# Kernel tuning notes

Hardware: AMD Instinct MI355X
Metric: run time of the kernel (lower is better)

Reference implementation:

```python
import jax, jax.numpy as jnp
import numpy as np

# ---- constants from the module ----
E_L, E_e, E_i = -65.0, 0.0, -80.0
V_th, V_reset, V_floor = -50.0, -65.0, -200.0
dt = 0.25
T_STEPS = 4000
DECAY_AMPA = float(np.exp(-dt / 2.0))   # tau_ampa = 2.0
DECAY_GABA = float(np.exp(-dt / 9.0))   # tau_gaba = 9.0
C_M_E, G_L_E = 1.0, 1.0 / 20.0          # tau_m_E = 20
C_M_I, G_L_I = 0.5, 0.5 / 5.0           # tau_m_I = 5
REF_E = 12                               # round(3.0/0.25)
REF_I = 6                                # round(1.5/0.25)
CM_BACK = 80.0
SLOPE = 1.0                              # biophysical surrogate slope

@jax.custom_vjp
def spike(u):
    # Heaviside forward, fast-sigmoid surrogate backward (SurrogateSpike)
    return (u >= 0).astype(u.dtype)

def _spike_fwd(u):
    return (u >= 0).astype(u.dtype), u

def _spike_bwd(u, g):
    return (g * SLOPE / (1.0 + SLOPE * jnp.abs(u)) ** 2,)

spike.defvjp(_spike_fwd, _spike_bwd)

def _scale_grad(x, scale):
    # forward identity, gradient scaled by `scale`
    return x * scale + jax.lax.stop_gradient(x) * (1.0 - scale)

def lif_step(v, I_total, ref, C_m, g_L, ref_steps):
    dv = (dt / C_m) * (-g_L * (v - E_L) + I_total)
    dv = _scale_grad(dv, 1.0 / CM_BACK)
    v = jnp.maximum(v + dv, V_floor)
    ref = jnp.maximum(ref - 1, 0)
    can_spike = ref == 0
    s = spike(v - V_th) * can_spike.astype(v.dtype)
    spiked_or_ref = (s > 0) | ~can_spike
    v = jnp.where(spiked_or_ref, V_reset, v)
    ref = jnp.where(s > 0, ref_steps, ref)
    return v, s, ref

def setup_inputs() -> dict:
    key = jax.random.key(0)
    ks = jax.random.split(key, 6)
    T, B, N_IN, N_E, N_I, N_OUT = T_STEPS, 64, 64, 256, 64, 10

    def init_w(k, shape, mean, std):
        # init_weight: N(mean,std) clamped >=0, fan-in normalized
        w = jnp.maximum(jax.random.normal(k, shape, jnp.float32) * std + mean, 0.0)
        return w / shape[0]

    return {
        "input_spikes": (jax.random.uniform(ks[0], (T, B, N_IN)) < 0.02).astype(jnp.float32),
        "W_ff0": init_w(ks[1], (N_IN, N_E), 5.1, 3.8),
        "W_ff1": init_w(ks[2], (N_E, N_OUT), 5.1, 3.8),
        "W_ee": init_w(ks[3], (N_E, N_E), 0.0, 0.0),
        "W_ei": init_w(ks[4], (N_E, N_I), 1.0, 0.5),
        "W_ie": init_w(ks[5], (N_I, N_E), 3.0, 1.5),
    }

def reference(input_spikes, W_ff0, W_ff1, W_ee, W_ei, W_ie):
    # Dale's law: feedforward weights clamped >= 0 in forward
    W0 = jnp.maximum(W_ff0, 0.0)
    W1 = jnp.maximum(W_ff1, 0.0)
    B = input_spikes.shape[1]
    N_E, N_I, N_OUT = W0.shape[1], W_ei.shape[1], W1.shape[1]
    f32 = input_spikes.dtype

    z = lambda n: jnp.zeros((B, n), f32)
    vl = lambda n: jnp.full((B, n), E_L, f32)
    zr = lambda n: jnp.zeros((B, n), jnp.int32)

    carry0 = (vl(N_E), zr(N_E), z(N_E), z(N_E), z(N_E),   # E pop: v, ref, g_ampa, g_gaba, spikes
              vl(N_I), zr(N_I), z(N_I), z(N_I),           # I pop: v, ref, g_ampa, spikes
              vl(N_OUT), zr(N_OUT), z(N_OUT),             # out pop: v, ref, g_ampa
              z(N_OUT))                                    # output spike accumulator

    def step(c, s_in):
        v_e, r_e, ge_e, gi_e, s_e, v_i, r_i, ge_i, s_i, v_o, r_o, g_o, acc = c
        # exp_synapse: spike kicks first, then decay
        ge_e = (ge_e + s_in @ W0 + s_e @ W_ee) * DECAY_AMPA
        gi_e = (gi_e + s_i @ W_ie) * DECAY_GABA
        ge_i = (ge_i + s_e @ W_ei) * DECAY_AMPA
        # E neurons: COBA with excitation + inhibition
        v_e, s_e, r_e = lif_step(v_e, ge_e * (E_e - v_e) + gi_e * (E_i - v_e), r_e, C_M_E, G_L_E, REF_E)
        # I neurons: COBA excitation only
        v_i, s_i, r_i = lif_step(v_i, ge_i * (E_e - v_i), r_i, C_M_I, G_L_I, REF_I)
        # output layer driven by fresh E spikes
        g_o = (g_o + s_e @ W1) * DECAY_AMPA
        v_o, s_o, r_o = lif_step(v_o, g_o * (E_e - v_o), r_o, C_M_E, G_L_E, REF_E)
        acc = acc + s_o
        return (v_e, r_e, ge_e, gi_e, s_e, v_i, r_i, ge_i, s_i, v_o, r_o, g_o, acc), None

    cT, _ = jax.lax.scan(step, carry0, input_spikes)
    return cT[-1]  # [B, N_OUT] output spike counts over T_steps
```

## Files before the change

### kernel.cpp

```cpp
#include <hip/hip_runtime.h>
#include <math.h>

#pragma clang fp contract(off)

#define BB 64
#define N_IN 64
#define N_E 256
#define N_I 64
#define N_OUT 10

__device__ inline unsigned long long rfl64(unsigned long long x) {
  unsigned int lo = __builtin_amdgcn_readfirstlane((unsigned int)x);
  unsigned int hi = __builtin_amdgcn_readfirstlane((unsigned int)(x >> 32));
  return (((unsigned long long)hi) << 32) | (unsigned long long)lo;
}

__global__ __launch_bounds__(256, 1) void ping_kernel(
    const float* __restrict__ g_in,
    const float* __restrict__ g_W0,
    const float* __restrict__ g_W1,
    const float* __restrict__ g_Wee,
    const float* __restrict__ g_Wei,
    const float* __restrict__ g_Wie,
    float* __restrict__ g_out,
    int T, float dA, float dG)
{
  const int tid  = threadIdx.x;
  const int lane = tid & 63;
  const int wav  = tid >> 6;
  const int b    = blockIdx.x;
  const int col  = (lane < N_OUT) ? lane : 0;

  __shared__ float sWie[N_I * N_E];
  __shared__ float sWei[N_E * N_I];
  __shared__ float sW1[N_E * N_OUT];
  __shared__ float sZeroRow[256];
  __shared__ float sP[2][4][64];
  __shared__ float sKo[2][4][16];
  __shared__ unsigned sTag[2][4];
  __shared__ unsigned long long sME[2][4];
  __shared__ int sWee;

  {
    const float4* s0 = (const float4*)g_Wie; float4* d0 = (float4*)sWie;
    for (int k = tid; k < (N_I * N_E) / 4; k += 256) d0[k] = s0[k];
    const float4* s1 = (const float4*)g_Wei; float4* d1 = (float4*)sWei;
    for (int k = tid; k < (N_E * N_I) / 4; k += 256) d1[k] = s1[k];
    for (int k = tid; k < N_E * N_OUT; k += 256) sW1[k] = fmaxf(g_W1[k], 0.f);
  }
  sZeroRow[tid] = 0.f;
  if (tid < 4) { sME[0][tid] = 0ull; sME[1][tid] = 0ull; }
  if (tid < 8) sTag[tid >> 2][tid & 3] = 0u;
  if (tid == 0) sWee = 0;
  {
    bool any = false;
    const float4* p = (const float4*)g_Wee;
    for (int k = tid; k < (N_E * N_E) / 4; k += 256) {
      float4 x = p[k];
      any |= (x.x != 0.f) | (x.y != 0.f) | (x.z != 0.f) | (x.w != 0.f);
    }
    if (__ballot(any) != 0ull && lane == 0) sWee = 1;
  }
  __syncthreads();
  const int wee = sWee;

  float vE = -65.f, ge = 0.f, gi = 0.f; int rE = 0;
  float vI = -65.f, gI = 0.f; int rI = 0;
  float vO = -65.f, gO = 0.f, accO = 0.f; int rO = 0;

  unsigned long long mE = 0ull;
  unsigned long long mI = 0ull;
  unsigned long long we0 = 0ull, we1 = 0ull, we2 = 0ull, we3 = 0ull;

  float cur = g_in[b * N_IN + lane];
  float n1  = g_in[((T > 1 ? 1 : 0) * BB + b) * N_IN + lane];

  unsigned long long mInC = __ballot(cur != 0.f);
  unsigned long long aRemC = 0ull;
  bool vaC[4] = {false, false, false, false};
  float fwC[4];
  if (mInC) {
    unsigned long long a = mInC;
    int ja[4];
#pragma unroll
    for (int k = 0; k < 4; ++k) {
      vaC[k] = (a != 0ull); ja[k] = vaC[k] ? (__ffsll(a) - 1) : 0; a &= (a - 1ull);
    }
    aRemC = a;
#pragma unroll
    for (int k = 0; k < 4; ++k) fwC[k] = g_W0[ja[k] * N_E + tid];
  }

  for (int t = 0; t < T; ++t) {
    const int slot = t & 1;
    const int tp = (t + 2 < T) ? (t + 2) : (T - 1);
    float n2 = g_in[(tp * BB + b) * N_IN + lane];

    float pEI = 0.f, kow = 0.f;
    {
      unsigned long long e = mE;
      const int base = wav * 64;
      while (e) {
        const float *qb[4], *rb[4];
#pragma unroll
        for (int k = 0; k < 4; ++k) {
          bool v = (e != 0ull); int j = v ? (__ffsll(e) - 1) : 0; e &= (e - 1ull);
          qb[k] = v ? &sWei[(base + j) * N_I] : sZeroRow;
          rb[k] = v ? &sW1[(base + j) * N_OUT] : sZeroRow;
        }
        float fq[4], fr[4];
#pragma unroll
        for (int k = 0; k < 4; ++k) { fq[k] = qb[k][lane]; fr[k] = rb[k][col]; }
#pragma unroll
        for (int k = 0; k < 4; ++k) pEI += fq[k];
#pragma unroll
        for (int k = 0; k < 4; ++k) kow += fr[k];
      }
    }

    sP[slot][wav][lane] = pEI;
    if (lane < 16) sKo[slot][wav][lane] = kow;
    asm volatile("s_waitcnt lgkmcnt(0)" ::: "memory");
    if (lane == 0) *((volatile unsigned*)&sTag[slot][wav]) = (unsigned)(t + 1);

    float kie = 0.f;
    {
      unsigned long long c = mI;
      while (c) {
        const float* pb[8];
#pragma unroll
        for (int k = 0; k < 8; ++k) {
          bool v = (c != 0ull); int j = v ? (__ffsll(c) - 1) : 0; c &= (c - 1ull);
          pb[k] = v ? &sWie[j * N_E] : sZeroRow;
        }
        float fI[8];
#pragma unroll
        for (int k = 0; k < 8; ++k) fI[k] = pb[k][tid];
#pragma unroll
        for (int k = 0; k < 8; ++k) kie += fI[k];
      }
    }

    float kin = 0.f;
    if (mInC) {
#pragma unroll
      for (int k = 0; k < 4; ++k) kin += vaC[k] ? fmaxf(fwC[k], 0.f) : 0.f;
      while (aRemC) {
        int j = __ffsll(aRemC) - 1; aRemC &= (aRemC - 1ull);
        kin += fmaxf(g_W0[j * N_E + tid], 0.f);
      }
    }

    float kee = 0.f;
    if (wee) {
      unsigned long long m0 = we0, m1 = we1, m2 = we2, m3 = we3;
      while (m0 | m1 | m2 | m3) {
        bool h0 = (m0 != 0ull), h1 = (m1 != 0ull), h2 = (m2 != 0ull), h3 = (m3 != 0ull);
        int idx = 0;
        if (h0)      { idx = __ffsll(m0) - 1;       m0 &= (m0 - 1ull); }
        else if (h1) { idx = 64 + __ffsll(m1) - 1;  m1 &= (m1 - 1ull); }
        else if (h2) { idx = 128 + __ffsll(m2) - 1; m2 &= (m2 - 1ull); }
        else if (h3) { idx = 192 + __ffsll(m3) - 1; m3 &= (m3 - 1ull); }
        kee += g_Wee[idx * N_E + tid];
      }
    }

    ge = ((ge + kin) + kee) * dA;
    gi = (gi + kie) * dG;
    {
      float t2 = ge * (0.f - vE);
      float t3 = gi * (-80.f - vE);
      float Itot = t2 + t3;
      float dv = 0.25f * ((-0.05f) * (vE - (-65.f)) + Itot);
      dv = dv * 0.0125f + dv * 0.9875f;
      vE = fmaxf(vE + dv, -200.f);
      rE = rE - 1; if (rE < 0) rE = 0;
      bool can = (rE == 0);
      bool sE = ((vE - (-50.f)) >= 0.f) && can;
      vE = (sE || !can) ? -65.f : vE;
      rE = sE ? 12 : rE;
      unsigned long long fresh = __ballot(sE);
      if (wee && lane == 0) sME[slot][wav] = fresh;
      mE = fresh;
    }

    {
      const unsigned want = (unsigned)(t + 1);
      volatile unsigned* vt = &sTag[slot][0];
      while (true) {
        unsigned a0 = vt[0], a1 = vt[1], a2 = vt[2], a3 = vt[3];
        if ((((a0 ^ want) | (a1 ^ want)) | ((a2 ^ want) | (a3 ^ want))) == 0u) break;
      }
      asm volatile("" ::: "memory");
    }

    float p0 = sP[slot][0][lane], p1 = sP[slot][1][lane];
    float p2 = sP[slot][2][lane], p3 = sP[slot][3][lane];
    float k0 = sKo[slot][0][col], k1 = sKo[slot][1][col];
    float k2 = sKo[slot][2][col], k3 = sKo[slot][3][col];

    {
      float p = ((p0 + p1) + p2) + p3;
      gI = (gI + p) * dA;
      float Ii = gI * (0.f - vI);
      float dvi = 0.5f * ((-0.1f) * (vI - (-65.f)) + Ii);
      dvi = dvi * 0.0125f + dvi * 0.9875f;
      vI = fmaxf(vI + dvi, -200.f);
      rI = rI - 1; if (rI < 0) rI = 0;
      bool canI = (rI == 0);
      bool sI = ((vI - (-50.f)) >= 0.f) && canI;
      vI = (sI || !canI) ? -65.f : vI;
      rI = sI ? 6 : rI;
      mI = __ballot(sI);
    }

    {
      float ko = ((k0 + k1) + k2) + k3;
      gO = (gO + ko) * dA;
      float Io = gO * (0.f - vO);
      float dvo = 0.25f * ((-0.05f) * (vO - (-65.f)) + Io);
      dvo = dvo * 0.0125f + dvo * 0.9875f;
      vO = fmaxf(vO + dvo, -200.f);
      rO = rO - 1; if (rO < 0) rO = 0;
      bool canO = (rO == 0);
      bool sO = ((vO - (-50.f)) >= 0.f) && canO;
      vO = (sO || !canO) ? -65.f : vO;
      rO = sO ? 12 : rO;
      accO += sO ? 1.f : 0.f;
    }

    if (wee) {
      __syncthreads();
      we0 = rfl64(sME[slot][0]); we1 = rfl64(sME[slot][1]);
      we2 = rfl64(sME[slot][2]); we3 = rfl64(sME[slot][3]);
    }

    mInC = __ballot(n1 != 0.f);
    aRemC = 0ull;
    vaC[0] = vaC[1] = vaC[2] = vaC[3] = false;
    if (mInC) {
      unsigned long long a = mInC;
      int ja[4];
#pragma unroll
      for (int k = 0; k < 4; ++k) {
        vaC[k] = (a != 0ull); ja[k] = vaC[k] ? (__ffsll(a) - 1) : 0; a &= (a - 1ull);
      }
      aRemC = a;
#pragma unroll
      for (int k = 0; k < 4; ++k) fwC[k] = g_W0[ja[k] * N_E + tid];
    }

    cur = n1; n1 = n2;
  }

  {
    float kd = 0.f;
    unsigned long long e = mE;
    const int base = wav * 64;
    while (e) {
      const float* rb[4];
#pragma unroll
      for (int k = 0; k < 4; ++k) {
        bool v = (e != 0ull); int j = v ? (__ffsll(e) - 1) : 0; e &= (e - 1ull);
        rb[k] = v ? &sW1[(base + j) * N_OUT] : sZeroRow;
      }
      float fr[4];
#pragma unroll
      for (int k = 0; k < 4; ++k) fr[k] = rb[k][col];
#pragma unroll
      for (int k = 0; k < 4; ++k) kd += fr[k];
    }
    __syncthreads();
    sP[0][wav][lane] = kd;
    __syncthreads();
    float ko = ((sP[0][0][col] + sP[0][1][col]) + sP[0][2][col]) + sP[0][3][col];
    gO = (gO + ko) * dA;
    float Io = gO * (0.f - vO);
    float dvo = 0.25f * ((-0.05f) * (vO - (-65.f)) + Io);
    dvo = dvo * 0.0125f + dvo * 0.9875f;
    vO = fmaxf(vO + dvo, -200.f);
    rO = rO - 1; if (rO < 0) rO = 0;
    bool canO = (rO == 0);
    bool sO = ((vO - (-50.f)) >= 0.f) && canO;
    accO += sO ? 1.f : 0.f;
  }

  if (wav == 0 && lane < N_OUT) g_out[b * N_OUT + lane] = accO;
}

extern "C" void kernel_launch(void* const* d_in, const int* in_sizes, int n_in,
                              void* d_out, int out_size, void* d_ws, size_t ws_size,
                              hipStream_t stream) {
  const float* g_in  = (const float*)d_in[0];
  const float* g_W0  = (const float*)d_in[1];
  const float* g_W1  = (const float*)d_in[2];
  const float* g_Wee = (const float*)d_in[3];
  const float* g_Wei = (const float*)d_in[4];
  const float* g_Wie = (const float*)d_in[5];
  float* out = (float*)d_out;
  int T = in_sizes[0] / (BB * N_IN);
  float dA = (float)exp(-0.25 / 2.0);
  float dG = (float)exp(-0.25 / 9.0);
  ping_kernel<<<dim3(BB), dim3(256), 0, stream>>>(g_in, g_W0, g_W1, g_Wee, g_Wei, g_Wie, out, T, dA, dG);
}
```

Before: 5.295 ms.

## Software-pipeline E-spike and I-spike LDS gathers into the previous iteration

Moves the gathers of Wei/W1 rows for fresh E spikes and of Wie rows for fresh I spikes so they are issued right after the spike ballots, overlapping the LDS latency with the inter-wave spin wait and the remaining neuron updates. The partial sums are carried across iterations (pEI_nx, kow_nx, kieF) and published at the start of the next step. The input-spike W0 prefetch is also moved earlier. This raises register pressure and changes the order of the float additions for pEI, which could shift results in rare cases.

```diff
diff --git a/kernel.cpp b/kernel.cpp
--- a/kernel.cpp
+++ b/kernel.cpp
@@ -72,6 +72,10 @@
   unsigned long long mI = 0ull;
   unsigned long long we0 = 0ull, we1 = 0ull, we2 = 0ull, we3 = 0ull;
 
+  float pEI_nx = 0.f, kow_nx = 0.f;
+  float kieF[8] = {0,0,0,0,0,0,0,0};
+  unsigned long long kieRem = 0ull;
+
   float cur = g_in[b * N_IN + lane];
   float n1  = g_in[((T > 1 ? 1 : 0) * BB + b) * N_IN + lane];
 
@@ -96,49 +100,26 @@
     const int tp = (t + 2 < T) ? (t + 2) : (T - 1);
     float n2 = g_in[(tp * BB + b) * N_IN + lane];
 
-    float pEI = 0.f, kow = 0.f;
-    {
-      unsigned long long e = mE;
-      const int base = wav * 64;
-      while (e) {
-        const float *qb[4], *rb[4];
-#pragma unroll
-        for (int k = 0; k < 4; ++k) {
-          bool v = (e != 0ull); int j = v ? (__ffsll(e) - 1) : 0; e &= (e - 1ull);
-          qb[k] = v ? &sWei[(base + j) * N_I] : sZeroRow;
-          rb[k] = v ? &sW1[(base + j) * N_OUT] : sZeroRow;
-        }
-        float fq[4], fr[4];
-#pragma unroll
-        for (int k = 0; k < 4; ++k) { fq[k] = qb[k][lane]; fr[k] = rb[k][col]; }
-#pragma unroll
-        for (int k = 0; k < 4; ++k) pEI += fq[k];
-#pragma unroll
-        for (int k = 0; k < 4; ++k) kow += fr[k];
-      }
-    }
-
-    sP[slot][wav][lane] = pEI;
-    if (lane < 16) sKo[slot][wav][lane] = kow;
+    sP[slot][wav][lane] = pEI_nx;
+    if (lane < 16) sKo[slot][wav][lane] = kow_nx;
     asm volatile("s_waitcnt lgkmcnt(0)" ::: "memory");
     if (lane == 0) *((volatile unsigned*)&sTag[slot][wav]) = (unsigned)(t + 1);
 
     float kie = 0.f;
-    {
-      unsigned long long c = mI;
-      while (c) {
-        const float* pb[8];
-#pragma unroll
-        for (int k = 0; k < 8; ++k) {
-          bool v = (c != 0ull); int j = v ? (__ffsll(c) - 1) : 0; c &= (c - 1ull);
-          pb[k] = v ? &sWie[j * N_E] : sZeroRow;
-        }
-        float fI[8];
-#pragma unroll
-        for (int k = 0; k < 8; ++k) fI[k] = pb[k][tid];
-#pragma unroll
-        for (int k = 0; k < 8; ++k) kie += fI[k];
-      }
+#pragma unroll
+    for (int k = 0; k < 8; ++k) kie += kieF[k];
+    while (kieRem) {
+      const float* pb[4];
+#pragma unroll
+      for (int k = 0; k < 4; ++k) {
+        bool v = (kieRem != 0ull); int j = v ? (__ffsll(kieRem) - 1) : 0; kieRem &= (kieRem - 1ull);
+        pb[k] = v ? &sWie[j * N_E] : sZeroRow;
+      }
+      float fI[4];
+#pragma unroll
+      for (int k = 0; k < 4; ++k) fI[k] = pb[k][tid];
+#pragma unroll
+      for (int k = 0; k < 4; ++k) kie += fI[k];
     }
 
     float kin = 0.f;
@@ -184,6 +165,38 @@
       mE = fresh;
     }
 
+    float fqN[6], frN[6];
+    unsigned long long eRem;
+    {
+      unsigned long long e = mE;
+      const int base = wav * 64;
+      const float *qb[6], *rb[6];
+#pragma unroll
+      for (int k = 0; k < 6; ++k) {
+        bool v = (e != 0ull); int j = v ? (__ffsll(e) - 1) : 0; e &= (e - 1ull);
+        qb[k] = v ? &sWei[(base + j) * N_I] : sZeroRow;
+        rb[k] = v ? &sW1[(base + j) * N_OUT] : sZeroRow;
+      }
+      eRem = e;
+#pragma unroll
+      for (int k = 0; k < 6; ++k) { fqN[k] = qb[k][lane]; frN[k] = rb[k][col]; }
+    }
+
+    mInC = __ballot(n1 != 0.f);
+    aRemC = 0ull;
+    vaC[0] = vaC[1] = vaC[2] = vaC[3] = false;
+    if (mInC) {
+      unsigned long long a = mInC;
+      int ja[4];
+#pragma unroll
+      for (int k = 0; k < 4; ++k) {
+        vaC[k] = (a != 0ull); ja[k] = vaC[k] ? (__ffsll(a) - 1) : 0; a &= (a - 1ull);
+      }
+      aRemC = a;
+#pragma unroll
+      for (int k = 0; k < 4; ++k) fwC[k] = g_W0[ja[k] * N_E + tid];
+    }
+
     {
       const unsigned want = (unsigned)(t + 1);
       volatile unsigned* vt = &sTag[slot][0];
@@ -215,6 +228,19 @@
     }
 
     {
+      unsigned long long c = mI;
+      const float* pb[8];
+#pragma unroll
+      for (int k = 0; k < 8; ++k) {
+        bool v = (c != 0ull); int j = v ? (__ffsll(c) - 1) : 0; c &= (c - 1ull);
+        pb[k] = v ? &sWie[j * N_E] : sZeroRow;
+      }
+      kieRem = c;
+#pragma unroll
+      for (int k = 0; k < 8; ++k) kieF[k] = pb[k][tid];
+    }
+
+    {
       float ko = ((k0 + k1) + k2) + k3;
       gO = (gO + ko) * dA;
       float Io = gO * (0.f - vO);
@@ -235,19 +261,30 @@
       we2 = rfl64(sME[slot][2]); we3 = rfl64(sME[slot][3]);
     }
 
-    mInC = __ballot(n1 != 0.f);
-    aRemC = 0ull;
-    vaC[0] = vaC[1] = vaC[2] = vaC[3] = false;
-    if (mInC) {
-      unsigned long long a = mInC;
-      int ja[4];
-#pragma unroll
-      for (int k = 0; k < 4; ++k) {
-        vaC[k] = (a != 0ull); ja[k] = vaC[k] ? (__ffsll(a) - 1) : 0; a &= (a - 1ull);
-      }
-      aRemC = a;
-#pragma unroll
-      for (int k = 0; k < 4; ++k) fwC[k] = g_W0[ja[k] * N_E + tid];
+    {
+      float pe = 0.f, ko2 = 0.f;
+#pragma unroll
+      for (int k = 0; k < 6; ++k) pe += fqN[k];
+#pragma unroll
+      for (int k = 0; k < 6; ++k) ko2 += frN[k];
+      const int base = wav * 64;
+      while (eRem) {
+        const float *qb[4], *rb[4];
+#pragma unroll
+        for (int k = 0; k < 4; ++k) {
+          bool v = (eRem != 0ull); int j = v ? (__ffsll(eRem) - 1) : 0; eRem &= (eRem - 1ull);
+          qb[k] = v ? &sWei[(base + j) * N_I] : sZeroRow;
+          rb[k] = v ? &sW1[(base + j) * N_OUT] : sZeroRow;
+        }
+        float fq[4], fr[4];
+#pragma unroll
+        for (int k = 0; k < 4; ++k) { fq[k] = qb[k][lane]; fr[k] = rb[k][col]; }
+#pragma unroll
+        for (int k = 0; k < 4; ++k) pe += fq[k];
+#pragma unroll
+        for (int k = 0; k < 4; ++k) ko2 += fr[k];
+      }
+      pEI_nx = pe; kow_nx = ko2;
     }
 
     cur = n1; n1 = n2;
```

Result: slower. 5.990 ms (+13.1%).

## Interleave Wei and W1 rows in shared memory and specialize loop on Wee

Applied to the files above, without the earlier changes.

Merges the E→I and E→output weight tables into one padded 80-wide shared-memory row per excitatory neuron, so each spiking neuron's contributions come from a single computed row pointer. The time loop is split into two specialized versions depending on whether W_ee is nonzero, removing the per-step wee branches and the recurrent-E machinery in the common zero case. It also moves the next-input mask preparation ahead of the spin-wait and polls the four wave tags with two 64-bit loads instead of four 32-bit loads. Costs are duplicated code and a serial per-thread global-to-shared copy during setup instead of vectorized float4 copies.

```diff
diff --git a/kernel.cpp b/kernel.cpp
--- a/kernel.cpp
+++ b/kernel.cpp
@@ -30,23 +30,27 @@
   const int wav  = tid >> 6;
   const int b    = blockIdx.x;
   const int col  = (lane < N_OUT) ? lane : 0;
+  const int colO = 64 + col;
 
   __shared__ float sWie[N_I * N_E];
-  __shared__ float sWei[N_E * N_I];
-  __shared__ float sW1[N_E * N_OUT];
+  __shared__ float sWeiO[N_E * 80];
   __shared__ float sZeroRow[256];
   __shared__ float sP[2][4][64];
   __shared__ float sKo[2][4][16];
-  __shared__ unsigned sTag[2][4];
+  __shared__ __align__(16) unsigned sTag[2][4];
   __shared__ unsigned long long sME[2][4];
   __shared__ int sWee;
 
   {
     const float4* s0 = (const float4*)g_Wie; float4* d0 = (float4*)sWie;
     for (int k = tid; k < (N_I * N_E) / 4; k += 256) d0[k] = s0[k];
-    const float4* s1 = (const float4*)g_Wei; float4* d1 = (float4*)sWei;
-    for (int k = tid; k < (N_E * N_I) / 4; k += 256) d1[k] = s1[k];
-    for (int k = tid; k < N_E * N_OUT; k += 256) sW1[k] = fmaxf(g_W1[k], 0.f);
+    {
+      int j = tid;
+      float* row = &sWeiO[j * 80];
+      for (int c = 0; c < 64; ++c) row[c] = g_Wei[j * N_I + c];
+      for (int o = 0; o < N_OUT; ++o) row[64 + o] = fmaxf(g_W1[j * N_OUT + o], 0.f);
+      for (int c = 74; c < 80; ++c) row[c] = 0.f;
+    }
   }
   sZeroRow[tid] = 0.f;
   if (tid < 4) { sME[0][tid] = 0ull; sME[1][tid] = 0ull; }
@@ -70,7 +74,6 @@
 
   unsigned long long mE = 0ull;
   unsigned long long mI = 0ull;
-  unsigned long long we0 = 0ull, we1 = 0ull, we2 = 0ull, we3 = 0ull;
 
   float cur = g_in[b * N_IN + lane];
   float n1  = g_in[((T > 1 ? 1 : 0) * BB + b) * N_IN + lane];
@@ -91,182 +94,321 @@
     for (int k = 0; k < 4; ++k) fwC[k] = g_W0[ja[k] * N_E + tid];
   }
 
-  for (int t = 0; t < T; ++t) {
-    const int slot = t & 1;
-    const int tp = (t + 2 < T) ? (t + 2) : (T - 1);
-    float n2 = g_in[(tp * BB + b) * N_IN + lane];
-
-    float pEI = 0.f, kow = 0.f;
-    {
-      unsigned long long e = mE;
-      const int base = wav * 64;
-      while (e) {
-        const float *qb[4], *rb[4];
+  const int base64 = wav * 64;
+
+  if (!wee) {
+    for (int t = 0; t < T; ++t) {
+      const int slot = t & 1;
+      const int tp = (t + 2 < T) ? (t + 2) : (T - 1);
+      float n2 = g_in[(tp * BB + b) * N_IN + lane];
+
+      float pEI = 0.f, kow = 0.f;
+      {
+        unsigned long long e = mE;
+        while (e) {
+          const float* qb[4];
+#pragma unroll
+          for (int k = 0; k < 4; ++k) {
+            bool v = (e != 0ull); int j = v ? (__ffsll(e) - 1) : 0; e &= (e - 1ull);
+            qb[k] = v ? &sWeiO[(base64 + j) * 80] : sZeroRow;
+          }
+          float fq[4], fr[4];
+#pragma unroll
+          for (int k = 0; k < 4; ++k) { fq[k] = qb[k][lane]; fr[k] = qb[k][colO]; }
+#pragma unroll
+          for (int k = 0; k < 4; ++k) pEI += fq[k];
+#pragma unroll
+          for (int k = 0; k < 4; ++k) kow += fr[k];
+        }
+      }
+
+      sP[slot][wav][lane] = pEI;
+      if (lane < 16) sKo[slot][wav][lane] = kow;
+      asm volatile("s_waitcnt lgkmcnt(0)" ::: "memory");
+      if (lane == 0) *((volatile unsigned*)&sTag[slot][wav]) = (unsigned)(t + 1);
+
+      float kie = 0.f;
+      {
+        unsigned long long c = mI;
+        while (c) {
+          const float* pb[8];
+#pragma unroll
+          for (int k = 0; k < 8; ++k) {
+            bool v = (c != 0ull); int j = v ? (__ffsll(c) - 1) : 0; c &= (c - 1ull);
+            pb[k] = v ? &sWie[j * N_E] : sZeroRow;
+          }
+          float fI[8];
+#pragma unroll
+          for (int k = 0; k < 8; ++k) fI[k] = pb[k][tid];
+#pragma unroll
+          for (int k = 0; k < 8; ++k) kie += fI[k];
+        }
+      }
+
+      float kin = 0.f;
+      if (mInC) {
+#pragma unroll
+        for (int k = 0; k < 4; ++k) kin += vaC[k] ? fmaxf(fwC[k], 0.f) : 0.f;
+        while (aRemC) {
+          int j = __ffsll(aRemC) - 1; aRemC &= (aRemC - 1ull);
+          kin += fmaxf(g_W0[j * N_E + tid], 0.f);
+        }
+      }
+
+      ge = (ge + kin) * dA;
+      gi = (gi + kie) * dG;
+      {
+        float t2 = ge * (0.f - vE);
+        float t3 = gi * (-80.f - vE);
+        float Itot = t2 + t3;
+        float dv = 0.25f * ((-0.05f) * (vE - (-65.f)) + Itot);
+        dv = dv * 0.0125f + dv * 0.9875f;
+        vE = fmaxf(vE + dv, -200.f);
+        rE = rE - 1; if (rE < 0) rE = 0;
+        bool can = (rE == 0);
+        bool sE = ((vE - (-50.f)) >= 0.f) && can;
+        vE = (sE || !can) ? -65.f : vE;
+        rE = sE ? 12 : rE;
+        mE = __ballot(sE);
+      }
+
+      mInC = __ballot(n1 != 0.f);
+      aRemC = 0ull;
+      vaC[0] = vaC[1] = vaC[2] = vaC[3] = false;
+      if (mInC) {
+        unsigned long long a = mInC;
+        int ja[4];
 #pragma unroll
         for (int k = 0; k < 4; ++k) {
-          bool v = (e != 0ull); int j = v ? (__ffsll(e) - 1) : 0; e &= (e - 1ull);
-          qb[k] = v ? &sWei[(base + j) * N_I] : sZeroRow;
-          rb[k] = v ? &sW1[(base + j) * N_OUT] : sZeroRow;
-        }
-        float fq[4], fr[4];
-#pragma unroll
-        for (int k = 0; k < 4; ++k) { fq[k] = qb[k][lane]; fr[k] = rb[k][col]; }
-#pragma unroll
-        for (int k = 0; k < 4; ++k) pEI += fq[k];
-#pragma unroll
-        for (int k = 0; k < 4; ++k) kow += fr[k];
-      }
-    }
-
-    sP[slot][wav][lane] = pEI;
-    if (lane < 16) sKo[slot][wav][lane] = kow;
-    asm volatile("s_waitcnt lgkmcnt(0)" ::: "memory");
-    if (lane == 0) *((volatile unsigned*)&sTag[slot][wav]) = (unsigned)(t + 1);
-
-    float kie = 0.f;
-    {
-      unsigned long long c = mI;
-      while (c) {
-        const float* pb[8];
-#pragma unroll
-        for (int k = 0; k < 8; ++k) {
-          bool v = (c != 0ull); int j = v ? (__ffsll(c) - 1) : 0; c &= (c - 1ull);
-          pb[k] = v ? &sWie[j * N_E] : sZeroRow;
-        }
-        float fI[8];
-#pragma unroll
-        for (int k = 0; k < 8; ++k) fI[k] = pb[k][tid];
-#pragma unroll
-        for (int k = 0; k < 8; ++k) kie += fI[k];
-      }
-    }
-
-    float kin = 0.f;
-    if (mInC) {
-#pragma unroll
-      for (int k = 0; k < 4; ++k) kin += vaC[k] ? fmaxf(fwC[k], 0.f) : 0.f;
-      while (aRemC) {
-        int j = __ffsll(aRemC) - 1; aRemC &= (aRemC - 1ull);
-        kin += fmaxf(g_W0[j * N_E + tid], 0.f);
-      }
-    }
-
-    float kee = 0.f;
-    if (wee) {
-      unsigned long long m0 = we0, m1 = we1, m2 = we2, m3 = we3;
-      while (m0 | m1 | m2 | m3) {
-        bool h0 = (m0 != 0ull), h1 = (m1 != 0ull), h2 = (m2 != 0ull), h3 = (m3 != 0ull);
-        int idx = 0;
-        if (h0)      { idx = __ffsll(m0) - 1;       m0 &= (m0 - 1ull); }
-        else if (h1) { idx = 64 + __ffsll(m1) - 1;  m1 &= (m1 - 1ull); }
-        else if (h2) { idx = 128 + __ffsll(m2) - 1; m2 &= (m2 - 1ull); }
-        else if (h3) { idx = 192 + __ffsll(m3) - 1; m3 &= (m3 - 1ull); }
-        kee += g_Wee[idx * N_E + tid];
-      }
-    }
-
-    ge = ((ge + kin) + kee) * dA;
-    gi = (gi + kie) * dG;
-    {
-      float t2 = ge * (0.f - vE);
-      float t3 = gi * (-80.f - vE);
-      float Itot = t2 + t3;
-      float dv = 0.25f * ((-0.05f) * (vE - (-65.f)) + Itot);
-      dv = dv * 0.0125f + dv * 0.9875f;
-      vE = fmaxf(vE + dv, -200.f);
-      rE = rE - 1; if (rE < 0) rE = 0;
-      bool can = (rE == 0);
-      bool sE = ((vE - (-50.f)) >= 0.f) && can;
-      vE = (sE || !can) ? -65.f : vE;
-      rE = sE ? 12 : rE;
-      unsigned long long fresh = __ballot(sE);
-      if (wee && lane == 0) sME[slot][wav] = fresh;
-      mE = fresh;
-    }
-
-    {
-      const unsigned want = (unsigned)(t + 1);
-      volatile unsigned* vt = &sTag[slot][0];
-      while (true) {
-        unsigned a0 = vt[0], a1 = vt[1], a2 = vt[2], a3 = vt[3];
-        if ((((a0 ^ want) | (a1 ^ want)) | ((a2 ^ want) | (a3 ^ want))) == 0u) break;
-      }
-      asm volatile("" ::: "memory");
-    }
-
-    float p0 = sP[slot][0][lane], p1 = sP[slot][1][lane];
-    float p2 = sP[slot][2][lane], p3 = sP[slot][3][lane];
-    float k0 = sKo[slot][0][col], k1 = sKo[slot][1][col];
-    float k2 = sKo[slot][2][col], k3 = sKo[slot][3][col];
-
-    {
-      float p = ((p0 + p1) + p2) + p3;
-      gI = (gI + p) * dA;
-      float Ii = gI * (0.f - vI);
-      float dvi = 0.5f * ((-0.1f) * (vI - (-65.f)) + Ii);
-      dvi = dvi * 0.0125f + dvi * 0.9875f;
-      vI = fmaxf(vI + dvi, -200.f);
-      rI = rI - 1; if (rI < 0) rI = 0;
-      bool canI = (rI == 0);
-      bool sI = ((vI - (-50.f)) >= 0.f) && canI;
-      vI = (sI || !canI) ? -65.f : vI;
-      rI = sI ? 6 : rI;
-      mI = __ballot(sI);
-    }
-
-    {
-      float ko = ((k0 + k1) + k2) + k3;
-      gO = (gO + ko) * dA;
-      float Io = gO * (0.f - vO);
-      float dvo = 0.25f * ((-0.05f) * (vO - (-65.f)) + Io);
-      dvo = dvo * 0.0125f + dvo * 0.9875f;
-      vO = fmaxf(vO + dvo, -200.f);
-      rO = rO - 1; if (rO < 0) rO = 0;
-      bool canO = (rO == 0);
-      bool sO = ((vO - (-50.f)) >= 0.f) && canO;
-      vO = (sO || !canO) ? -65.f : vO;
-      rO = sO ? 12 : rO;
-      accO += sO ? 1.f : 0.f;
-    }
-
-    if (wee) {
+          vaC[k] = (a != 0ull); ja[k] = vaC[k] ? (__ffsll(a) - 1) : 0; a &= (a - 1ull);
+        }
+        aRemC = a;
+#pragma unroll
+        for (int k = 0; k < 4; ++k) fwC[k] = g_W0[ja[k] * N_E + tid];
+      }
+
+      {
+        const unsigned want = (unsigned)(t + 1);
+        const unsigned long long want2 = (((unsigned long long)want) << 32) | want;
+        volatile unsigned long long* vt = (volatile unsigned long long*)&sTag[slot][0];
+        while (true) {
+          unsigned long long a0 = vt[0], a1 = vt[1];
+          if (((a0 ^ want2) | (a1 ^ want2)) == 0ull) break;
+        }
+        asm volatile("" ::: "memory");
+      }
+
+      float p0 = sP[slot][0][lane], p1 = sP[slot][1][lane];
+      float p2 = sP[slot][2][lane], p3 = sP[slot][3][lane];
+      float k0 = sKo[slot][0][col], k1 = sKo[slot][1][col];
+      float k2 = sKo[slot][2][col], k3 = sKo[slot][3][col];
+
+      {
+        float p = ((p0 + p1) + p2) + p3;
+        gI = (gI + p) * dA;
+        float Ii = gI * (0.f - vI);
+        float dvi = 0.5f * ((-0.1f) * (vI - (-65.f)) + Ii);
+        dvi = dvi * 0.0125f + dvi * 0.9875f;
+        vI = fmaxf(vI + dvi, -200.f);
+        rI = rI - 1; if (rI < 0) rI = 0;
+        bool canI = (rI == 0);
+        bool sI = ((vI - (-50.f)) >= 0.f) && canI;
+        vI = (sI || !canI) ? -65.f : vI;
+        rI = sI ? 6 : rI;
+        mI = __ballot(sI);
+      }
+
+      {
+        float ko = ((k0 + k1) + k2) + k3;
+        gO = (gO + ko) * dA;
+        float Io = gO * (0.f - vO);
+        float dvo = 0.25f * ((-0.05f) * (vO - (-65.f)) + Io);
+        dvo = dvo * 0.0125f + dvo * 0.9875f;
+        vO = fmaxf(vO + dvo, -200.f);
+        rO = rO - 1; if (rO < 0) rO = 0;
+        bool canO = (rO == 0);
+        bool sO = ((vO - (-50.f)) >= 0.f) && canO;
+        vO = (sO || !canO) ? -65.f : vO;
+        rO = sO ? 12 : rO;
+        accO += sO ? 1.f : 0.f;
+      }
+
+      cur = n1; n1 = n2;
+    }
+  } else {
+    unsigned long long we0 = 0ull, we1 = 0ull, we2 = 0ull, we3 = 0ull;
+    for (int t = 0; t < T; ++t) {
+      const int slot = t & 1;
+      const int tp = (t + 2 < T) ? (t + 2) : (T - 1);
+      float n2 = g_in[(tp * BB + b) * N_IN + lane];
+
+      float pEI = 0.f, kow = 0.f;
+      {
+        unsigned long long e = mE;
+        while (e) {
+          const float* qb[4];
+#pragma unroll
+          for (int k = 0; k < 4; ++k) {
+            bool v = (e != 0ull); int j = v ? (__ffsll(e) - 1) : 0; e &= (e - 1ull);
+            qb[k] = v ? &sWeiO[(base64 + j) * 80] : sZeroRow;
+          }
+          float fq[4], fr[4];
+#pragma unroll
+          for (int k = 0; k < 4; ++k) { fq[k] = qb[k][lane]; fr[k] = qb[k][colO]; }
+#pragma unroll
+          for (int k = 0; k < 4; ++k) pEI += fq[k];
+#pragma unroll
+          for (int k = 0; k < 4; ++k) kow += fr[k];
+        }
+      }
+      sP[slot][wav][lane] = pEI;
+      if (lane < 16) sKo[slot][wav][lane] = kow;
+      asm volatile("s_waitcnt lgkmcnt(0)" ::: "memory");
+      if (lane == 0) *((volatile unsigned*)&sTag[slot][wav]) = (unsigned)(t + 1);
+
+      float kie = 0.f;
+      {
+        unsigned long long c = mI;
+        while (c) {
+          const float* pb[8];
+#pragma unroll
+          for (int k = 0; k < 8; ++k) {
+            bool v = (c != 0ull); int j = v ? (__ffsll(c) - 1) : 0; c &= (c - 1ull);
+            pb[k] = v ? &sWie[j * N_E] : sZeroRow;
+          }
+          float fI[8];
+#pragma unroll
+          for (int k = 0; k < 8; ++k) fI[k] = pb[k][tid];
+#pragma unroll
+          for (int k = 0; k < 8; ++k) kie += fI[k];
+        }
+      }
+
+      float kin = 0.f;
+      if (mInC) {
+#pragma unroll
+        for (int k = 0; k < 4; ++k) kin += vaC[k] ? fmaxf(fwC[k], 0.f) : 0.f;
+        while (aRemC) {
+          int j = __ffsll(aRemC) - 1; aRemC &= (aRemC - 1ull);
+          kin += fmaxf(g_W0[j * N_E + tid], 0.f);
+        }
+      }
+
+      float kee = 0.f;
+      {
+        unsigned long long m0 = we0, m1 = we1, m2 = we2, m3 = we3;
+        while (m0 | m1 | m2 | m3) {
+          bool h0 = (m0 != 0ull), h1 = (m1 != 0ull), h2 = (m2 != 0ull), h3 = (m3 != 0ull);
+          int idx = 0;
+          if (h0)      { idx = __ffsll(m0) - 1;       m0 &= (m0 - 1ull); }
+          else if (h1) { idx = 64 + __ffsll(m1) - 1;  m1 &= (m1 - 1ull); }
+          else if (h2) { idx = 128 + __ffsll(m2) - 1; m2 &= (m2 - 1ull); }
+          else if (h3) { idx = 192 + __ffsll(m3) - 1; m3 &= (m3 - 1ull); }
+          kee += g_Wee[idx * N_E + tid];
+        }
+      }
+
+      ge = ((ge + kin) + kee) * dA;
+      gi = (gi + kie) * dG;
+      {
+        float t2 = ge * (0.f - vE);
+        float t3 = gi * (-80.f - vE);
+        float Itot = t2 + t3;
+        float dv = 0.25f * ((-0.05f) * (vE - (-65.f)) + Itot);
+        dv = dv * 0.0125f + dv * 0.9875f;
+        vE = fmaxf(vE + dv, -200.f);
+        rE = rE - 1; if (rE < 0) rE = 0;
+        bool can = (rE == 0);
+        bool sE = ((vE - (-50.f)) >= 0.f) && can;
+        vE = (sE || !can) ? -65.f : vE;
+        rE = sE ? 12 : rE;
+        unsigned long long fresh = __ballot(sE);
+        if (lane == 0) sME[slot][wav] = fresh;
+        mE = fresh;
+      }
+
+      mInC = __ballot(n1 != 0.f);
+      aRemC = 0ull;
+      vaC[0] = vaC[1] = vaC[2] = vaC[3] = false;
+      if (mInC) {
+        unsigned long long a = mInC;
+        int ja[4];
+#pragma unroll
+        for (int k = 0; k < 4; ++k) {
+          vaC[k] = (a != 0ull); ja[k] = vaC[k] ? (__ffsll(a) - 1) : 0; a &= (a - 1ull);
+        }
+        aRemC = a;
+#pragma unroll
+        for (int k = 0; k < 4; ++k) fwC[k] = g_W0[ja[k] * N_E + tid];
+      }
+
+      {
+        const unsigned want = (unsigned)(t + 1);
+        const unsigned long long want2 = (((unsigned long long)want) << 32) | want;
+        volatile unsigned long long* vt = (volatile unsigned long long*)&sTag[slot][0];
+        while (true) {
+          unsigned long long a0 = vt[0], a1 = vt[1];
+          if (((a0 ^ want2) | (a1 ^ want2)) == 0ull) break;
+        }
+        asm volatile("" ::: "memory");
+      }
+
+      float p0 = sP[slot][0][lane], p1 = sP[slot][1][lane];
+      float p2 = sP[slot][2][lane], p3 = sP[slot][3][lane];
+      float k0 = sKo[slot][0][col], k1 = sKo[slot][1][col];
+      float k2 = sKo[slot][2][col], k3 = sKo[slot][3][col];
+
+      {
+        float p = ((p0 + p1) + p2) + p3;
+        gI = (gI + p) * dA;
+        float Ii = gI * (0.f - vI);
+        float dvi = 0.5f * ((-0.1f) * (vI - (-65.f)) + Ii);
+        dvi = dvi * 0.0125f + dvi * 0.9875f;
+        vI = fmaxf(vI + dvi, -200.f);
+        rI = rI - 1; if (rI < 0) rI = 0;
+        bool canI = (rI == 0);
+        bool sI = ((vI - (-50.f)) >= 0.f) && canI;
+        vI = (sI || !canI) ? -65.f : vI;
+        rI = sI ? 6 : rI;
+        mI = __ballot(sI);
+      }
+
+      {
+        float ko = ((k0 + k1) + k2) + k3;
+        gO = (gO + ko) * dA;
+        float Io = gO * (0.f - vO);
+        float dvo = 0.25f * ((-0.05f) * (vO - (-65.f)) + Io);
+        dvo = dvo * 0.0125f + dvo * 0.9875f;
+        vO = fmaxf(vO + dvo, -200.f);
+        rO = rO - 1; if (rO < 0) rO = 0;
+        bool canO = (rO == 0);
+        bool sO = ((vO - (-50.f)) >= 0.f) && canO;
+        vO = (sO || !canO) ? -65.f : vO;
+        rO = sO ? 12 : rO;
+        accO += sO ? 1.f : 0.f;
+      }
+
       __syncthreads();
       we0 = rfl64(sME[slot][0]); we1 = rfl64(sME[slot][1]);
       we2 = rfl64(sME[slot][2]); we3 = rfl64(sME[slot][3]);
-    }
-
-    mInC = __ballot(n1 != 0.f);
-    aRemC = 0ull;
-    vaC[0] = vaC[1] = vaC[2] = vaC[3] = false;
-    if (mInC) {
-      unsigned long long a = mInC;
-      int ja[4];
-#pragma unroll
-      for (int k = 0; k < 4; ++k) {
-        vaC[k] = (a != 0ull); ja[k] = vaC[k] ? (__ffsll(a) - 1) : 0; a &= (a - 1ull);
-      }
-      aRemC = a;
-#pragma unroll
-      for (int k = 0; k < 4; ++k) fwC[k] = g_W0[ja[k] * N_E + tid];
-    }
-
-    cur = n1; n1 = n2;
+
+      cur = n1; n1 = n2;
+    }
   }
 
   {
     float kd = 0.f;
     unsigned long long e = mE;
-    const int base = wav * 64;
     while (e) {
       const float* rb[4];
 #pragma unroll
       for (int k = 0; k < 4; ++k) {
         bool v = (e != 0ull); int j = v ? (__ffsll(e) - 1) : 0; e &= (e - 1ull);
-        rb[k] = v ? &sW1[(base + j) * N_OUT] : sZeroRow;
+        rb[k] = v ? &sWeiO[(base64 + j) * 80] : sZeroRow;
       }
       float fr[4];
 #pragma unroll
-      for (int k = 0; k < 4; ++k) fr[k] = rb[k][col];
+      for (int k = 0; k < 4; ++k) fr[k] = rb[k][colO];
 #pragma unroll
       for (int k = 0; k < 4; ++k) kd += fr[k];
     }
```

Result: faster. 4.891 ms (-7.6%).
